# Kernel tuning notes

Hardware: AMD Instinct MI355X
Metric: run time of the kernel (lower is better)

Reference implementation:

```python
import jax, jax.numpy as jnp
import numpy as np

N = 65536        # flattened ray-sample count
K = 8            # net_kernels (experts)
WID = 64         # net_width
D = 32           # feature dim (num_output_channels)
POS_DEG = 2
VIEW_DEG = 4
DIN = D + (3 + 2 * POS_DEG * 3) + (3 + 2 * VIEW_DEG * 3)  # 74


def posenc(x, deg):
    # coord.pos_enc with min_deg=0, max_deg=deg, append_identity=True
    scales = 2.0 ** jnp.arange(deg, dtype=x.dtype)            # [deg]
    xb = (x[..., None, :] * scales[:, None]).reshape(*x.shape[:-1], deg * x.shape[-1])
    four = jnp.sin(jnp.concatenate([xb, xb + 0.5 * jnp.pi], axis=-1))
    return jnp.concatenate([x, four], axis=-1)


def multi_dense(idx, x, kernel, bias):
    # per-sample expert gather + small matmul: x [N,din], kernel [K,din,dout]
    w = kernel[idx]                                           # [N,din,dout]
    return jnp.einsum('ni,nio->no', x, w) + bias[idx]


def _he_uniform(key, shape):
    fan_in = shape[-2]
    lim = np.sqrt(6.0 / fan_in).astype(np.float32)
    return jax.random.uniform(key, shape, jnp.float32, -lim, lim)


def setup_inputs() -> dict:
    key = jax.random.key(0)
    ks = jax.random.split(key, 8)
    idxs = jax.random.randint(ks[0], (N, 1), 0, K, dtype=jnp.int32)
    positions = jax.random.normal(ks[1], (N, 3), jnp.float32)
    viewdirs = jax.random.normal(ks[2], (N, 3), jnp.float32)
    viewdirs = viewdirs / jnp.linalg.norm(viewdirs, axis=-1, keepdims=True)
    features = jax.random.normal(ks[3], (N, D), jnp.float32)
    W0 = _he_uniform(ks[4], (K, DIN, WID))
    b0 = jnp.zeros((K, WID), jnp.float32)
    W1 = _he_uniform(ks[5], (K, WID, WID))
    b1 = jnp.zeros((K, WID), jnp.float32)
    W2 = _he_uniform(ks[6], (K, WID, D))
    b2 = jnp.zeros((K, D), jnp.float32)
    return {'idxs': idxs, 'positions': positions, 'viewdirs': viewdirs,
            'features': features, 'W0': W0, 'b0': b0, 'W1': W1, 'b1': b1,
            'W2': W2, 'b2': b2}


def reference(idxs, positions, viewdirs, features, W0, b0, W1, b1, W2, b2):
    idx = idxs.reshape(-1)                                    # [N]
    x = jnp.concatenate([features,
                         posenc(positions, POS_DEG),
                         posenc(viewdirs, VIEW_DEG)], axis=-1)  # [N, DIN]
    h = jax.nn.relu(multi_dense(idx, x, W0, b0))              # [N, WID]
    h = jax.nn.relu(multi_dense(idx, h, W1, b1))              # [N, WID]
    return multi_dense(idx, h, W2, b2)                        # [N, D]
```

## Files before the change

### kernel.cpp

```cpp
#include <hip/hip_runtime.h>
#include <hip/hip_bf16.h>

#define NS    65536
#define KEXP  8
#define WID   64
#define DOUT  32
#define DIN   74
#define TM    64
#define XS    104
#define HS    72
#define OSF   36
#define GX    64
#define HDR   32768

typedef __attribute__((ext_vector_type(8))) short short8;
typedef __attribute__((ext_vector_type(4))) float floatx4;

__device__ __forceinline__ unsigned short f2b(float f) {
  unsigned u = __builtin_bit_cast(unsigned, f);
  u = u + 0x7FFFu + ((u >> 16) & 1u);
  return (unsigned short)(u >> 16);
}


__global__ void k_zero(int* __restrict__ hdr) {
  if (threadIdx.x < KEXP) hdr[threadIdx.x] = 0;
}

__global__ __launch_bounds__(256) void k_count(const int* __restrict__ idxs,
                                               int* __restrict__ hdr) {
  __shared__ int lc[KEXP];
  const int tid = threadIdx.x;
  if (tid < KEXP) lc[tid] = 0;
  __syncthreads();
  const int e = idxs[blockIdx.x * 256 + tid];
  atomicAdd(&lc[e], 1);
  __syncthreads();
  if (tid < KEXP) atomicAdd(&hdr[tid], lc[tid]);
}

__global__ void k_scan(int* __restrict__ hdr) {
  if (threadIdx.x == 0) {
    int acc = 0;
    for (int e = 0; e < KEXP; ++e) {
      hdr[8 + e] = acc;
      hdr[16 + e] = acc;
      acc += hdr[e];
    }
  }
}

__global__ __launch_bounds__(256) void k_scatter(const int* __restrict__ idxs,
                                                 int* __restrict__ hdr,
                                                 unsigned short* __restrict__ bucket) {
  __shared__ int lc[KEXP];
  __shared__ int lbase[KEXP];
  const int tid = threadIdx.x;
  if (tid < KEXP) lc[tid] = 0;
  __syncthreads();
  const int gid = blockIdx.x * 256 + tid;
  const int e = idxs[gid];
  const int rank = atomicAdd(&lc[e], 1);
  __syncthreads();
  if (tid < KEXP) lbase[tid] = atomicAdd(&hdr[16 + tid], lc[tid]);
  __syncthreads();
  bucket[lbase[e] + rank] = (unsigned short)gid;
}

__global__ __launch_bounds__(256) void k_mlp(
    const int* __restrict__ hdr,
    const unsigned short* __restrict__ bucket,
    const float* __restrict__ pos,
    const float* __restrict__ view,
    const float* __restrict__ feat,
    const float* __restrict__ W0,
    const float* __restrict__ B0,
    const float* __restrict__ W1,
    const float* __restrict__ B1,
    const float* __restrict__ W2,
    const float* __restrict__ B2,
    float* __restrict__ out)
{
  const int e = blockIdx.y;
  const int segCnt = hdr[e];
  if ((int)blockIdx.x * TM >= segCnt) return;
  const int segStart = hdr[8 + e];
  const int tid = threadIdx.x;

  __shared__ __align__(16) unsigned short Xs[TM * XS];
  __shared__ __align__(16) unsigned short W0t[WID * XS];
  __shared__ __align__(16) unsigned short W1t[WID * HS];
  __shared__ __align__(16) unsigned short W2t[DOUT * HS];
  __shared__ __align__(16) unsigned short Hs[TM * HS];
  __shared__ __align__(16) float Os[TM * OSF];
  __shared__ float sb0[WID];
  __shared__ float sb1[WID];
  __shared__ float sb2[DOUT];
  __shared__ int sid[TM];

  for (int i = tid; i < TM * XS; i += 256) Xs[i] = 0;
  for (int i = tid; i < WID * XS; i += 256) W0t[i] = 0;
  __syncthreads();

  {
    const float* g0 = W0 + (size_t)e * DIN * WID;
    for (int g = tid; g < DIN * WID; g += 256) {
      int i = g >> 6, o = g & 63;
      W0t[o * XS + i] = f2b(g0[g]);
    }
    const float* g1 = W1 + (size_t)e * WID * WID;
    for (int g = tid; g < WID * WID; g += 256) {
      int i = g >> 6, o = g & 63;
      W1t[o * HS + i] = f2b(g1[g]);
    }
    const float* g2 = W2 + (size_t)e * WID * DOUT;
    for (int g = tid; g < WID * DOUT; g += 256) {
      int i = g >> 5, o = g & 31;
      W2t[o * HS + i] = f2b(g2[g]);
    }
    if (tid < WID) {
      sb0[tid] = B0[e * WID + tid];
      sb1[tid] = B1[e * WID + tid];
    } else if (tid < WID + DOUT) {
      int t = tid - WID;
      sb2[t] = B2[e * DOUT + t];
    }
  }
  __syncthreads();

  const int lane = tid & 63;
  const int wv = tid >> 6;
  const int quad = lane >> 4;
  const int r16 = lane & 15;
  const int rb = wv * 16;

  for (int tile = blockIdx.x; tile * TM < segCnt; tile += GX) {
    const int t0 = tile * TM;
    const int rows = min(TM, segCnt - t0);

    const int r = lane;
    if (r < rows) {
      const int s = (int)bucket[segStart + t0 + r];
      unsigned short* xr = &Xs[r * XS];
      if (wv == 0) {
        sid[r] = s;
        const float4* fs = (const float4*)(feat + (size_t)s * DOUT);
        #pragma unroll
        for (int q = 0; q < 4; ++q) {
          float4 f = fs[q];
          xr[q * 4 + 0] = f2b(f.x);
          xr[q * 4 + 1] = f2b(f.y);
          xr[q * 4 + 2] = f2b(f.z);
          xr[q * 4 + 3] = f2b(f.w);
        }
      } else if (wv == 1) {
        const float4* fs = (const float4*)(feat + (size_t)s * DOUT);
        #pragma unroll
        for (int q = 4; q < 8; ++q) {
          float4 f = fs[q];
          xr[q * 4 + 0] = f2b(f.x);
          xr[q * 4 + 1] = f2b(f.y);
          xr[q * 4 + 2] = f2b(f.z);
          xr[q * 4 + 3] = f2b(f.w);
        }
      } else if (wv == 2) {
        float p[3];
        p[0] = pos[s * 3 + 0];
        p[1] = pos[s * 3 + 1];
        p[2] = pos[s * 3 + 2];
        #pragma unroll
        for (int d = 0; d < 3; ++d) xr[32 + d] = f2b(p[d]);
        #pragma unroll
        for (int si = 0; si < 2; ++si) {
          const float sc = (float)(1 << si);
          #pragma unroll
          for (int d = 0; d < 3; ++d) {
            const float a = p[d] * sc;
            xr[35 + si * 3 + d] = f2b(__sinf(a));
            xr[41 + si * 3 + d] = f2b(__cosf(a));
          }
        }
      } else {
        float v[3];
        v[0] = view[s * 3 + 0];
        v[1] = view[s * 3 + 1];
        v[2] = view[s * 3 + 2];
        #pragma unroll
        for (int d = 0; d < 3; ++d) xr[47 + d] = f2b(v[d]);
        #pragma unroll
        for (int si = 0; si < 4; ++si) {
          const float sc = (float)(1 << si);
          #pragma unroll
          for (int d = 0; d < 3; ++d) {
            const float a = v[d] * sc;
            xr[50 + si * 3 + d] = f2b(__sinf(a));
            xr[62 + si * 3 + d] = f2b(__cosf(a));
          }
        }
      }
    }
    __syncthreads();

    {
      const short8 a0 = *(const short8*)&Xs[(rb + r16) * XS + 0 + quad * 8];
      const short8 a1 = *(const short8*)&Xs[(rb + r16) * XS + 32 + quad * 8];
      const short8 a2 = *(const short8*)&Xs[(rb + r16) * XS + 64 + quad * 8];
      #pragma unroll
      for (int c = 0; c < 4; ++c) {
        const int n0 = c * 16;
        floatx4 acc = {0.f, 0.f, 0.f, 0.f};
        acc = __builtin_amdgcn_mfma_f32_16x16x32_bf16(
            a0, *(const short8*)&W0t[(n0 + r16) * XS + 0 + quad * 8], acc, 0, 0, 0);
        acc = __builtin_amdgcn_mfma_f32_16x16x32_bf16(
            a1, *(const short8*)&W0t[(n0 + r16) * XS + 32 + quad * 8], acc, 0, 0, 0);
        acc = __builtin_amdgcn_mfma_f32_16x16x32_bf16(
            a2, *(const short8*)&W0t[(n0 + r16) * XS + 64 + quad * 8], acc, 0, 0, 0);
        const float bias = sb0[n0 + r16];
        #pragma unroll
        for (int g = 0; g < 4; ++g) {
          const float vv = fmaxf(acc[g] + bias, 0.f);
          Hs[(rb + quad * 4 + g) * HS + n0 + r16] = f2b(vv);
        }
      }
    }
    __syncthreads();

    {
      const short8 h0 = *(const short8*)&Hs[(rb + r16) * HS + 0 + quad * 8];
      const short8 h1 = *(const short8*)&Hs[(rb + r16) * HS + 32 + quad * 8];
      __syncthreads();
      #pragma unroll
      for (int c = 0; c < 4; ++c) {
        const int n0 = c * 16;
        floatx4 acc = {0.f, 0.f, 0.f, 0.f};
        acc = __builtin_amdgcn_mfma_f32_16x16x32_bf16(
            h0, *(const short8*)&W1t[(n0 + r16) * HS + 0 + quad * 8], acc, 0, 0, 0);
        acc = __builtin_amdgcn_mfma_f32_16x16x32_bf16(
            h1, *(const short8*)&W1t[(n0 + r16) * HS + 32 + quad * 8], acc, 0, 0, 0);
        const float bias = sb1[n0 + r16];
        #pragma unroll
        for (int g = 0; g < 4; ++g) {
          const float vv = fmaxf(acc[g] + bias, 0.f);
          Hs[(rb + quad * 4 + g) * HS + n0 + r16] = f2b(vv);
        }
      }
    }
    __syncthreads();

    {
      const short8 q0 = *(const short8*)&Hs[(rb + r16) * HS + 0 + quad * 8];
      const short8 q1 = *(const short8*)&Hs[(rb + r16) * HS + 32 + quad * 8];
      #pragma unroll
      for (int c = 0; c < 2; ++c) {
        const int n0 = c * 16;
        floatx4 acc = {0.f, 0.f, 0.f, 0.f};
        acc = __builtin_amdgcn_mfma_f32_16x16x32_bf16(
            q0, *(const short8*)&W2t[(n0 + r16) * HS + 0 + quad * 8], acc, 0, 0, 0);
        acc = __builtin_amdgcn_mfma_f32_16x16x32_bf16(
            q1, *(const short8*)&W2t[(n0 + r16) * HS + 32 + quad * 8], acc, 0, 0, 0);
        const float bias = sb2[n0 + r16];
        #pragma unroll
        for (int g = 0; g < 4; ++g) {
          Os[(rb + quad * 4 + g) * OSF + n0 + r16] = acc[g] + bias;
        }
      }
    }
    __syncthreads();

    if (tid < rows) {
      const int s = sid[tid];
      float4* dst = (float4*)(out + (size_t)s * DOUT);
      const float4* src = (const float4*)&Os[tid * OSF];
      #pragma unroll
      for (int q = 0; q < 8; ++q) dst[q] = src[q];
    }
    __syncthreads();
  }
}

extern "C" void kernel_launch(void* const* d_in, const int* in_sizes, int n_in,
                              void* d_out, int out_size, void* d_ws, size_t ws_size,
                              hipStream_t stream) {
  const int* idxs        = (const int*)d_in[0];
  const float* pos       = (const float*)d_in[1];
  const float* view      = (const float*)d_in[2];
  const float* feat      = (const float*)d_in[3];
  const float* W0        = (const float*)d_in[4];
  const float* b0        = (const float*)d_in[5];
  const float* W1        = (const float*)d_in[6];
  const float* b1        = (const float*)d_in[7];
  const float* W2        = (const float*)d_in[8];
  const float* b2        = (const float*)d_in[9];
  float* out             = (float*)d_out;
  unsigned short* bucket = (unsigned short*)d_ws;
  int* hdr               = (int*)d_ws + HDR;

  k_zero<<<1, 64, 0, stream>>>(hdr);
  k_count<<<NS / 256, 256, 0, stream>>>(idxs, hdr);
  k_scan<<<1, 64, 0, stream>>>(hdr);
  k_scatter<<<NS / 256, 256, 0, stream>>>(idxs, hdr, bucket);
  dim3 grid(GX, KEXP);
  k_mlp<<<grid, 256, 0, stream>>>(hdr, bucket, pos, view, feat,
                                  W0, b0, W1, b1, W2, b2, out);
}
```

Before: 107.9 us.

## Drop count/scan kernels via fixed-capacity buckets and trim MLP syncs

Replaces the zero, count and scan kernels with a memset plus fixed per-expert bucket regions of capacity 65536, so a single scatter kernel both counts and places samples. In the MLP kernel, weight transposes now write 4 packed bf16 values per store, several block barriers are removed because each wave only reads Hs rows it wrote itself, and the output is written straight from MFMA accumulators instead of staging through shared memory. This cuts launches and LDS traffic, but the direct output stores are scattered 4-byte writes instead of float4 rows. Workspace use also grows to 1 MB of buckets.

```diff
diff --git a/kernel.cpp b/kernel.cpp
--- a/kernel.cpp
+++ b/kernel.cpp
@@ -9,9 +9,8 @@
 #define TM    64
 #define XS    104
 #define HS    72
-#define OSF   36
 #define GX    64
-#define HDR   32768
+#define SEGCAP 65536
 
 typedef __attribute__((ext_vector_type(8))) short short8;
 typedef __attribute__((ext_vector_type(4))) float floatx4;
@@ -23,35 +22,8 @@
 }
 
 
-__global__ void k_zero(int* __restrict__ hdr) {
-  if (threadIdx.x < KEXP) hdr[threadIdx.x] = 0;
-}
-
-__global__ __launch_bounds__(256) void k_count(const int* __restrict__ idxs,
-                                               int* __restrict__ hdr) {
-  __shared__ int lc[KEXP];
-  const int tid = threadIdx.x;
-  if (tid < KEXP) lc[tid] = 0;
-  __syncthreads();
-  const int e = idxs[blockIdx.x * 256 + tid];
-  atomicAdd(&lc[e], 1);
-  __syncthreads();
-  if (tid < KEXP) atomicAdd(&hdr[tid], lc[tid]);
-}
-
-__global__ void k_scan(int* __restrict__ hdr) {
-  if (threadIdx.x == 0) {
-    int acc = 0;
-    for (int e = 0; e < KEXP; ++e) {
-      hdr[8 + e] = acc;
-      hdr[16 + e] = acc;
-      acc += hdr[e];
-    }
-  }
-}
-
 __global__ __launch_bounds__(256) void k_scatter(const int* __restrict__ idxs,
-                                                 int* __restrict__ hdr,
+                                                 int* __restrict__ cursors,
                                                  unsigned short* __restrict__ bucket) {
   __shared__ int lc[KEXP];
   __shared__ int lbase[KEXP];
@@ -62,13 +34,13 @@
   const int e = idxs[gid];
   const int rank = atomicAdd(&lc[e], 1);
   __syncthreads();
-  if (tid < KEXP) lbase[tid] = atomicAdd(&hdr[16 + tid], lc[tid]);
-  __syncthreads();
-  bucket[lbase[e] + rank] = (unsigned short)gid;
+  if (tid < KEXP) lbase[tid] = atomicAdd(&cursors[tid], lc[tid]);
+  __syncthreads();
+  bucket[(e << 16) + lbase[e] + rank] = (unsigned short)gid;
 }
 
 __global__ __launch_bounds__(256) void k_mlp(
-    const int* __restrict__ hdr,
+    const int* __restrict__ cursors,
     const unsigned short* __restrict__ bucket,
     const float* __restrict__ pos,
     const float* __restrict__ view,
@@ -82,9 +54,9 @@
     float* __restrict__ out)
 {
   const int e = blockIdx.y;
-  const int segCnt = hdr[e];
+  const int segCnt = cursors[e];
   if ((int)blockIdx.x * TM >= segCnt) return;
-  const int segStart = hdr[8 + e];
+  const int segStart = e << 16;
   const int tid = threadIdx.x;
 
   __shared__ __align__(16) unsigned short Xs[TM * XS];
@@ -92,7 +64,6 @@
   __shared__ __align__(16) unsigned short W1t[WID * HS];
   __shared__ __align__(16) unsigned short W2t[DOUT * HS];
   __shared__ __align__(16) unsigned short Hs[TM * HS];
-  __shared__ __align__(16) float Os[TM * OSF];
   __shared__ float sb0[WID];
   __shared__ float sb1[WID];
   __shared__ float sb2[DOUT];
@@ -104,25 +75,39 @@
 
   {
     const float* g0 = W0 + (size_t)e * DIN * WID;
-    for (int g = tid; g < DIN * WID; g += 256) {
-      int i = g >> 6, o = g & 63;
-      W0t[o * XS + i] = f2b(g0[g]);
+    for (int g = tid; g < 19 * WID; g += 256) {
+      const int o = g & 63, i4 = g >> 6, ib = i4 * 4;
+      unsigned v0 = 0, v1 = 0;
+      #pragma unroll
+      for (int j = 0; j < 4; ++j) {
+        const int i = ib + j;
+        unsigned short w = (i < DIN) ? f2b(g0[i * WID + o]) : (unsigned short)0;
+        if (j < 2) v0 |= (unsigned)w << (16 * j);
+        else       v1 |= (unsigned)w << (16 * (j - 2));
+      }
+      *(uint2*)&W0t[o * XS + ib] = make_uint2(v0, v1);
     }
     const float* g1 = W1 + (size_t)e * WID * WID;
-    for (int g = tid; g < WID * WID; g += 256) {
-      int i = g >> 6, o = g & 63;
-      W1t[o * HS + i] = f2b(g1[g]);
+    for (int g = tid; g < 16 * WID; g += 256) {
+      const int o = g & 63, i4 = g >> 6, ib = i4 * 4;
+      unsigned v0, v1;
+      v0 = (unsigned)f2b(g1[(ib + 0) * WID + o]) | ((unsigned)f2b(g1[(ib + 1) * WID + o]) << 16);
+      v1 = (unsigned)f2b(g1[(ib + 2) * WID + o]) | ((unsigned)f2b(g1[(ib + 3) * WID + o]) << 16);
+      *(uint2*)&W1t[o * HS + ib] = make_uint2(v0, v1);
     }
     const float* g2 = W2 + (size_t)e * WID * DOUT;
-    for (int g = tid; g < WID * DOUT; g += 256) {
-      int i = g >> 5, o = g & 31;
-      W2t[o * HS + i] = f2b(g2[g]);
+    for (int g = tid; g < 16 * DOUT; g += 256) {
+      const int o = g & 31, i4 = g >> 5, ib = i4 * 4;
+      unsigned v0, v1;
+      v0 = (unsigned)f2b(g2[(ib + 0) * DOUT + o]) | ((unsigned)f2b(g2[(ib + 1) * DOUT + o]) << 16);
+      v1 = (unsigned)f2b(g2[(ib + 2) * DOUT + o]) | ((unsigned)f2b(g2[(ib + 3) * DOUT + o]) << 16);
+      *(uint2*)&W2t[o * HS + ib] = make_uint2(v0, v1);
     }
     if (tid < WID) {
       sb0[tid] = B0[e * WID + tid];
       sb1[tid] = B1[e * WID + tid];
     } else if (tid < WID + DOUT) {
-      int t = tid - WID;
+      const int t = tid - WID;
       sb2[t] = B2[e * DOUT + t];
     }
   }
@@ -137,6 +122,8 @@
   for (int tile = blockIdx.x; tile * TM < segCnt; tile += GX) {
     const int t0 = tile * TM;
     const int rows = min(TM, segCnt - t0);
+
+    __syncthreads();
 
     const int r = lane;
     if (r < rows) {
@@ -223,12 +210,10 @@
         }
       }
     }
-    __syncthreads();
 
     {
       const short8 h0 = *(const short8*)&Hs[(rb + r16) * HS + 0 + quad * 8];
       const short8 h1 = *(const short8*)&Hs[(rb + r16) * HS + 32 + quad * 8];
-      __syncthreads();
       #pragma unroll
       for (int c = 0; c < 4; ++c) {
         const int n0 = c * 16;
@@ -245,7 +230,6 @@
         }
       }
     }
-    __syncthreads();
 
     {
       const short8 q0 = *(const short8*)&Hs[(rb + r16) * HS + 0 + quad * 8];
@@ -259,22 +243,16 @@
         acc = __builtin_amdgcn_mfma_f32_16x16x32_bf16(
             q1, *(const short8*)&W2t[(n0 + r16) * HS + 32 + quad * 8], acc, 0, 0, 0);
         const float bias = sb2[n0 + r16];
+        const int col = n0 + r16;
         #pragma unroll
         for (int g = 0; g < 4; ++g) {
-          Os[(rb + quad * 4 + g) * OSF + n0 + r16] = acc[g] + bias;
-        }
-      }
-    }
-    __syncthreads();
-
-    if (tid < rows) {
-      const int s = sid[tid];
-      float4* dst = (float4*)(out + (size_t)s * DOUT);
-      const float4* src = (const float4*)&Os[tid * OSF];
-      #pragma unroll
-      for (int q = 0; q < 8; ++q) dst[q] = src[q];
-    }
-    __syncthreads();
+          const int row = rb + quad * 4 + g;
+          if (row < rows) {
+            out[(size_t)sid[row] * DOUT + col] = acc[g] + bias;
+          }
+        }
+      }
+    }
   }
 }
 
@@ -293,13 +271,11 @@
   const float* b2        = (const float*)d_in[9];
   float* out             = (float*)d_out;
   unsigned short* bucket = (unsigned short*)d_ws;
-  int* hdr               = (int*)d_ws + HDR;
-
-  k_zero<<<1, 64, 0, stream>>>(hdr);
-  k_count<<<NS / 256, 256, 0, stream>>>(idxs, hdr);
-  k_scan<<<1, 64, 0, stream>>>(hdr);
-  k_scatter<<<NS / 256, 256, 0, stream>>>(idxs, hdr, bucket);
+  int* cursors           = (int*)((char*)d_ws + (size_t)KEXP * SEGCAP * 2);
+
+  hipMemsetAsync(cursors, 0, KEXP * sizeof(int), stream);
+  k_scatter<<<NS / 256, 256, 0, stream>>>(idxs, cursors, bucket);
   dim3 grid(GX, KEXP);
-  k_mlp<<<grid, 256, 0, stream>>>(hdr, bucket, pos, view, feat,
+  k_mlp<<<grid, 256, 0, stream>>>(cursors, bucket, pos, view, feat,
                                   W0, b0, W1, b1, W2, b2, out);
 }
```

Result: faster. 104.0 us (-3.7%).
